# Kernel optimization log

Measured on AMD Instinct MI355X. Metric: run time of the kernel, lower is better.

Reference implementation:

```python
import jax, jax.numpy as jnp
import numpy as np

# ---- quantization scales (per-tensor, as produced by from_float calibration) ----
IN_SCALE = 0.05      # ForwardTokenizer: fp32 hidden -> int8
ALPHA_Q = 1e-4       # W8A8B8O8 requant multipliers (already include 1/sqrt(head_dim) for q)
ALPHA_K = 1e-4
ALPHA_V = 1e-4
QK_ALPHA = 1e-3      # BMM_S8T_S8N_F32T dequant scale (q_scale * k_scale)
PV_ALPHA = 1.0/127.0 # BMM_S8T_S8N_S8T requant scale ((1/127)*v_scale/out_scale)
OUT_ALPHA = 1e-4     # W8A8BFP32OFP32 dequant scale
NUM_HEADS = 32


def _quant_i8(x, scale):
    # simulate int8 quantization in fp32 (values are exact small integers)
    return jnp.clip(jnp.round(x / scale), -128.0, 127.0)


def _w8a8b8o8(x_i8, W_i8, b_i8, alpha):
    # int8 GEMM with int8 bias, requantized to int8: clamp(round(alpha*(x@W^T) + b))
    acc = jnp.einsum('btd,ed->bte', x_i8, W_i8)  # int32 accumulator in fp32
    return jnp.clip(jnp.round(alpha * acc + b_i8), -128.0, 127.0)


def setup_inputs() -> dict:
    key = jax.random.key(0)
    ks = jax.random.split(key, 10)
    B, T, D = 2, 2048, 2560
    hidden_states = jax.random.normal(ks[0], (B, T, D), dtype=jnp.float32)
    # causal additive mask, shape (B,1,T,T)
    neg = jnp.float32(-1e9)
    causal = jnp.where(jnp.tril(jnp.ones((T, T), dtype=bool)), 0.0, neg)
    attention_mask = jnp.broadcast_to(causal[None, None], (B, 1, T, T)).astype(jnp.float32)
    # int8-valued weights/biases stored as fp32 integers in [-127,127]
    def i8(k, shape):
        return jax.random.randint(k, shape, -127, 128).astype(jnp.float32)
    Wq = i8(ks[1], (D, D)); bq = i8(ks[2], (D,))
    Wk = i8(ks[3], (D, D)); bk = i8(ks[4], (D,))
    Wv = i8(ks[5], (D, D)); bv = i8(ks[6], (D,))
    Wo = i8(ks[7], (D, D))
    bo = jax.random.normal(ks[8], (D,), dtype=jnp.float32) * 0.01  # fp32 out bias
    return {"hidden_states": hidden_states, "attention_mask": attention_mask,
            "Wq": Wq, "bq": bq, "Wk": Wk, "bk": bk, "Wv": Wv, "bv": bv,
            "Wo": Wo, "bo": bo}


def reference(hidden_states, attention_mask, Wq, bq, Wk, bk, Wv, bv, Wo, bo):
    B, T, D = hidden_states.shape
    H = NUM_HEADS
    Dh = D // H
    # ForwardTokenizer: fp32 -> int8
    x_i8 = _quant_i8(hidden_states, IN_SCALE)
    # fused int8 q/k/v projections (W8A8B8O8Linear)
    q = _w8a8b8o8(x_i8, Wq, bq, ALPHA_Q)
    k = _w8a8b8o8(x_i8, Wk, bk, ALPHA_K)
    v = _w8a8b8o8(x_i8, Wv, bv, ALPHA_V)
    # (B,T,D) -> (B,H,T,Dh)
    def shape(t):
        return t.reshape(B, T, H, Dh).transpose(0, 2, 1, 3)
    q, k, v = shape(q), shape(k), shape(v)
    # BMM_S8T_S8N_F32T: int8 q @ k^T dequantized to fp32
    attn_weights = QK_ALPHA * jnp.einsum('bhqd,bhkd->bhqk', q, k)
    attn_weights = attn_weights + attention_mask  # (B,H,T,T)
    attn_weights = jnp.maximum(attn_weights, jnp.finfo(jnp.float32).min)
    attn_probs = jax.nn.softmax(attn_weights, axis=-1)
    # requantize probs to int8: mul_(127).round_()
    p_i8 = jnp.round(attn_probs * 127.0)
    # BMM_S8T_S8N_S8T: int8 p @ v requantized to int8
    attn_out = jnp.clip(jnp.round(PV_ALPHA * jnp.einsum('bhqk,bhkd->bhqd', p_i8, v)), -128.0, 127.0)
    # (B,H,T,Dh) -> (B,T,D)
    attn_out = attn_out.transpose(0, 2, 1, 3).reshape(B, T, D)
    # W8A8BFP32OFP32Linear: int8 GEMM, fp32 dequant + fp32 bias
    out = OUT_ALPHA * jnp.einsum('btd,ed->bte', attn_out, Wo) + bo
    return out
```

## Files before the change

kernel.cpp:

```cpp
#include <hip/hip_runtime.h>
#include <stdint.h>

typedef int v4i __attribute__((ext_vector_type(4)));

#define MFMA_I8(a,b,c) __builtin_amdgcn_mfma_i32_16x16x64_i8(a,b,c,0,0,0)

#define TD 2560
#define TT 2048
#define TB 2
#define TH 32
#define TDH 80
#define TDHP 128
#define TM 4096

#define LOG2E_MS 1.4426950408889634e-3f
#define MASKI (-(1<<30))
#define MAGICF 12582912.0f

__device__ __forceinline__ float clamp8f(float v){ return fminf(fmaxf(v, -128.0f), 127.0f); }
__device__ __forceinline__ float fexp2(float x){ return __builtin_amdgcn_exp2f(x); }

__device__ __forceinline__ void gl_lds16(const int8_t* g, int8_t* l){
  __builtin_amdgcn_global_load_lds(
      (const __attribute__((address_space(1))) void*)g,
      (__attribute__((address_space(3))) void*)l, 16, 0, 0);
}

__global__ void k_quant(const float* __restrict__ x, int8_t* __restrict__ y, int n4){
  int stride = gridDim.x * blockDim.x;
  for (int i = blockIdx.x*blockDim.x + threadIdx.x; i < n4; i += stride){
    float4 v = ((const float4*)x)[i];
    char4 o;
    o.x = (int8_t)clamp8f(rintf(__fdiv_rn(v.x, 0.05f)));
    o.y = (int8_t)clamp8f(rintf(__fdiv_rn(v.y, 0.05f)));
    o.z = (int8_t)clamp8f(rintf(__fdiv_rn(v.z, 0.05f)));
    o.w = (int8_t)clamp8f(rintf(__fdiv_rn(v.w, 0.05f)));
    ((char4*)y)[i] = o;
  }
}

__global__ void k_conv4(const float* __restrict__ w0, const float* __restrict__ w1,
                        const float* __restrict__ w2, const float* __restrict__ w3,
                        int8_t* __restrict__ y0, int8_t* __restrict__ y1,
                        int8_t* __restrict__ y2, int8_t* __restrict__ y3, int n4){
  const int z = blockIdx.y;
  const float* w = z == 0 ? w0 : (z == 1 ? w1 : (z == 2 ? w2 : w3));
  int8_t* y = z == 0 ? y0 : (z == 1 ? y1 : (z == 2 ? y2 : y3));
  int stride = gridDim.x * blockDim.x;
  for (int i = blockIdx.x*blockDim.x + threadIdx.x; i < n4; i += stride){
    float4 v = ((const float4*)w)[i];
    char4 o;
    o.x = (int8_t)(int)rintf(v.x);
    o.y = (int8_t)(int)rintf(v.y);
    o.z = (int8_t)(int)rintf(v.z);
    o.w = (int8_t)(int)rintf(v.w);
    ((char4*)y)[i] = o;
  }
}

__global__ __launch_bounds__(256, 4) void k_qkvg(const int8_t* __restrict__ x,
    const int8_t* __restrict__ w0_, const int8_t* __restrict__ w1_, const int8_t* __restrict__ w2_,
    const float* __restrict__ b0_, const float* __restrict__ b1_, const float* __restrict__ b2_,
    int8_t* __restrict__ dq, int8_t* __restrict__ dk, int8_t* __restrict__ dv)
{
  __shared__ __align__(16) int8_t As[128*64];
  __shared__ __align__(16) int8_t Bs[128*64];
  const int z = blockIdx.z;
  const int8_t* w = z == 0 ? w0_ : (z == 1 ? w1_ : w2_);
  const float* bias = z == 0 ? b0_ : (z == 1 ? b1_ : b2_);
  const int m0 = blockIdx.x * 128, n0 = blockIdx.y * 128;
  const int t = threadIdx.x;
  const int wv = t >> 6, l = t & 63, lhi = (l >> 4) & 3, llo = l & 15;
  const int wr = wv >> 1, wc = wv & 1;
  const int grow = l >> 2;
  const int gcol = ((l & 3) ^ ((l >> 3) & 3)) * 16;

  const int8_t* xa0 = x + (size_t)(m0 + wv*16 + grow)*TD + gcol;
  const int8_t* xa1 = x + (size_t)(m0 + 64 + wv*16 + grow)*TD + gcol;
  const int8_t* wb0 = w + (size_t)(n0 + wv*16 + grow)*TD + gcol;
  const int8_t* wb1 = w + (size_t)(n0 + 64 + wv*16 + grow)*TD + gcol;
  int8_t* la0 = &As[(wv*16)*64];
  int8_t* la1 = &As[(64 + wv*16)*64];
  int8_t* lb0 = &Bs[(wv*16)*64];
  int8_t* lb1 = &Bs[(64 + wv*16)*64];

  const int sca = (lhi ^ ((llo >> 1) & 3)) << 4;

  v4i acc[4][4] = {};
  for (int k0 = 0; k0 < TD; k0 += 64){
    gl_lds16(xa0 + k0, la0);
    gl_lds16(xa1 + k0, la1);
    gl_lds16(wb0 + k0, lb0);
    gl_lds16(wb1 + k0, lb1);
    __syncthreads();
    v4i a[4], b[4];
    #pragma unroll
    for (int mi = 0; mi < 4; ++mi)
      a[mi] = *(const v4i*)&As[(wr*64 + mi*16 + llo)*64 + sca];
    #pragma unroll
    for (int ni = 0; ni < 4; ++ni)
      b[ni] = *(const v4i*)&Bs[(wc*64 + ni*16 + llo)*64 + sca];
    #pragma unroll
    for (int mi = 0; mi < 4; ++mi)
      #pragma unroll
      for (int ni = 0; ni < 4; ++ni)
        acc[mi][ni] = MFMA_I8(a[mi], b[ni], acc[mi][ni]);
    __syncthreads();
  }

  #pragma unroll
  for (int mi = 0; mi < 4; ++mi)
  #pragma unroll
  for (int ni = 0; ni < 4; ++ni)
  #pragma unroll
  for (int r = 0; r < 4; ++r){
    int rowg = m0 + wr*64 + mi*16 + lhi*4 + r;
    int colg = n0 + wc*64 + ni*16 + llo;
    float fv = __fadd_rn(__fmul_rn(1e-4f, (float)acc[mi][ni][r]), bias[colg]);
    int8_t q8 = (int8_t)clamp8f(rintf(fv));
    int bb = rowg >> 11, tl = rowg & 2047;
    int hh = colg / 80, dh = colg - hh*80;
    if (z == 0)      dq[((size_t)(bb*TH + hh)*TT + tl)*TDHP + dh] = q8;
    else if (z == 1) dk[((size_t)(bb*TH + hh)*TT + tl)*TDHP + dh] = q8;
    else             dv[((size_t)(bb*TH + hh)*TDH + dh)*TT + tl] = q8;
  }
}

__global__ __launch_bounds__(256, 4) void k_oproj128(const int8_t* __restrict__ x,
    const int8_t* __restrict__ w, const float* __restrict__ bo,
    float* __restrict__ out)
{
  __shared__ __align__(16) int8_t As[128*64];
  __shared__ __align__(16) int8_t Bs[128*64];
  const int m0 = blockIdx.x * 128, n0 = blockIdx.y * 128;
  const int t = threadIdx.x;
  const int wv = t >> 6, l = t & 63, lhi = (l >> 4) & 3, llo = l & 15;
  const int wr = wv >> 1, wc = wv & 1;
  const int grow = l >> 2;
  const int gcol = ((l & 3) ^ ((l >> 3) & 3)) * 16;

  const int8_t* xa0 = x + (size_t)(m0 + wv*16 + grow)*TD + gcol;
  const int8_t* xa1 = x + (size_t)(m0 + 64 + wv*16 + grow)*TD + gcol;
  const int8_t* wb0 = w + (size_t)(n0 + wv*16 + grow)*TD + gcol;
  const int8_t* wb1 = w + (size_t)(n0 + 64 + wv*16 + grow)*TD + gcol;
  int8_t* la0 = &As[(wv*16)*64];
  int8_t* la1 = &As[(64 + wv*16)*64];
  int8_t* lb0 = &Bs[(wv*16)*64];
  int8_t* lb1 = &Bs[(64 + wv*16)*64];

  const int sca = (lhi ^ ((llo >> 1) & 3)) << 4;

  v4i acc[4][4] = {};
  for (int k0 = 0; k0 < TD; k0 += 64){
    gl_lds16(xa0 + k0, la0);
    gl_lds16(xa1 + k0, la1);
    gl_lds16(wb0 + k0, lb0);
    gl_lds16(wb1 + k0, lb1);
    __syncthreads();
    v4i a[4], b[4];
    #pragma unroll
    for (int mi = 0; mi < 4; ++mi)
      a[mi] = *(const v4i*)&As[(wr*64 + mi*16 + llo)*64 + sca];
    #pragma unroll
    for (int ni = 0; ni < 4; ++ni)
      b[ni] = *(const v4i*)&Bs[(wc*64 + ni*16 + llo)*64 + sca];
    #pragma unroll
    for (int mi = 0; mi < 4; ++mi)
      #pragma unroll
      for (int ni = 0; ni < 4; ++ni)
        acc[mi][ni] = MFMA_I8(a[mi], b[ni], acc[mi][ni]);
    __syncthreads();
  }

  #pragma unroll
  for (int mi = 0; mi < 4; ++mi)
  #pragma unroll
  for (int ni = 0; ni < 4; ++ni)
  #pragma unroll
  for (int r = 0; r < 4; ++r){
    int rowg = m0 + wr*64 + mi*16 + lhi*4 + r;
    int colg = n0 + wc*64 + ni*16 + llo;
    out[(size_t)rowg*TD + colg] =
        __fadd_rn(__fmul_rn(1e-4f, (float)acc[mi][ni][r]), bo[colg]);
  }
}

__global__ __launch_bounds__(256, 6) void k_attn6(const int8_t* __restrict__ qb_,
    const int8_t* __restrict__ kb_, const int8_t* __restrict__ vt_,
    int8_t* __restrict__ ao)
{
  __shared__ __align__(16) int8_t Ks[64*128];
  const int flat = blockIdx.x;
  const int g = flat & 7, ii = flat >> 3;
  const int qt = 31 - (ii >> 3);
  const int pair = g*8 + (ii & 7);
  const int h = pair & 31, b = pair >> 5;

  const int t = threadIdx.x, wv = t >> 6, l = t & 63, lhi = (l >> 4) & 3, llo = l & 15;
  const size_t bh = (size_t)(b*TH + h);
  const int8_t* qb = qb_ + bh*TT*TDHP;
  const int8_t* kb = kb_ + bh*TT*TDHP;
  const int8_t* vb = vt_ + bh*TDH*TT;

  const int qw0 = qt*64 + wv*16;
  const int qg = qw0 + llo;
  const int ktmax = qt + 1;

  int koff0[4], koff1[4];
  #pragma unroll
  for (int sub = 0; sub < 4; ++sub){
    const int row = sub*16 + llo, sw = row & 7;
    koff0[sub] = row*128 + (((lhi  ) ^ sw) << 4);
    koff1[sub] = row*128 + (((lhi+4) ^ sw) << 4);
  }

  v4i qa0 = *(const v4i*)(qb + (size_t)(qw0 + llo)*TDHP + lhi*16);
  v4i qa1 = {0,0,0,0};
  if (lhi == 0) qa1 = *(const v4i*)(qb + (size_t)(qw0 + llo)*TDHP + 64);

  const int srow = t >> 2, scp = (t & 3) * 2, ssw = srow & 7;
  const int8_t* kg = kb + (size_t)srow*TDHP + scp*16;
  int8_t* sdst0 = &Ks[srow*128 + (((scp  ) ^ ssw) << 4)];
  int8_t* sdst1 = &Ks[srow*128 + (((scp+1) ^ ssw) << 4)];

  int   M  = MASKI;
  float cm = __fmul_rn(LOG2E_MS, (float)MASKI);
  float ls = 0.0f;

  v4i pr0 = *(const v4i*)(kg);
  v4i pr1 = *(const v4i*)(kg + 16);
  *(v4i*)sdst0 = pr0; *(v4i*)sdst1 = pr1;
  for (int kt = 0; kt < ktmax; ++kt){
    if (kt + 1 < ktmax){
      pr0 = *(const v4i*)(kg + (size_t)(kt+1)*64*TDHP);
      pr1 = *(const v4i*)(kg + (size_t)(kt+1)*64*TDHP + 16);
    }
    __syncthreads();
    int sv[4][4];
    if (kt < qt){
      #pragma unroll
      for (int sub = 0; sub < 4; ++sub){
        v4i kf0 = *(const v4i*)&Ks[koff0[sub]];
        v4i kf1 = *(const v4i*)&Ks[koff1[sub]];
        v4i d = {}; d = MFMA_I8(kf0, qa0, d); d = MFMA_I8(kf1, qa1, d);
        sv[sub][0]=d[0]; sv[sub][1]=d[1]; sv[sub][2]=d[2]; sv[sub][3]=d[3];
      }
    } else {
      #pragma unroll
      for (int sub = 0; sub < 4; ++sub){
        if (sub <= wv){
          v4i kf0 = *(const v4i*)&Ks[koff0[sub]];
          v4i kf1 = *(const v4i*)&Ks[koff1[sub]];
          v4i d = {}; d = MFMA_I8(kf0, qa0, d); d = MFMA_I8(kf1, qa1, d);
          const int base = kt*64 + sub*16 + lhi*4;
          #pragma unroll
          for (int r = 0; r < 4; ++r)
            sv[sub][r] = (base + r <= qg) ? d[r] : MASKI;
        } else {
          #pragma unroll
          for (int r = 0; r < 4; ++r) sv[sub][r] = MASKI;
        }
      }
    }
    int m0 = max(max(sv[0][0], sv[0][1]), sv[0][2]);
    int m1 = max(max(sv[0][3], sv[1][0]), sv[1][1]);
    int m2 = max(max(sv[1][2], sv[1][3]), sv[2][0]);
    int m3 = max(max(sv[2][1], sv[2][2]), sv[2][3]);
    int m4 = max(max(sv[3][0], sv[3][1]), sv[3][2]);
    int tm = max(max(max(m0, m1), max(m2, m3)), max(m4, sv[3][3]));
    int Mn = max(M, tm);
    float cmN = __fmul_rn(LOG2E_MS, (float)Mn);
    float fac = fexp2(__fsub_rn(cm, cmN));
    float tot = 0.0f;
    #pragma unroll
    for (int sub = 0; sub < 4; ++sub){
      float e0 = fexp2(__fmaf_rn((float)sv[sub][0], LOG2E_MS, -cmN));
      float e1 = fexp2(__fmaf_rn((float)sv[sub][1], LOG2E_MS, -cmN));
      float e2 = fexp2(__fmaf_rn((float)sv[sub][2], LOG2E_MS, -cmN));
      float e3 = fexp2(__fmaf_rn((float)sv[sub][3], LOG2E_MS, -cmN));
      tot = __fadd_rn(tot, __fadd_rn(__fadd_rn(e0, e1), __fadd_rn(e2, e3)));
    }
    ls = __fmaf_rn(ls, fac, tot);
    M = Mn; cm = cmN;
    __syncthreads();
    if (kt + 1 < ktmax){ *(v4i*)sdst0 = pr0; *(v4i*)sdst1 = pr1; }
  }

  float rq;
  {
    float mm = cm, ll = ls;
    #pragma unroll
    for (int off = 16; off < 64; off <<= 1){
      float om = __shfl_xor(mm, off);
      float ol = __shfl_xor(ll, off);
      float mn = fmaxf(mm, om);
      ll = __fadd_rn(__fmul_rn(ll, fexp2(__fsub_rn(mm, mn))),
                     __fmul_rn(ol, fexp2(__fsub_rn(om, mn))));
      mm = mn;
    }
    cm = mm;
    rq = __fdiv_rn(127.0f, ll);
  }

  v4i pacc[5] = {};
  pr0 = *(const v4i*)(kg);
  pr1 = *(const v4i*)(kg + 16);
  __syncthreads();
  *(v4i*)sdst0 = pr0; *(v4i*)sdst1 = pr1;
  for (int kt = 0; kt < ktmax; ++kt){
    if (kt + 1 < ktmax){
      pr0 = *(const v4i*)(kg + (size_t)(kt+1)*64*TDHP);
      pr1 = *(const v4i*)(kg + (size_t)(kt+1)*64*TDHP + 16);
    }
    __syncthreads();
    uint32_t w[4] = {0u,0u,0u,0u};
    if (kt < qt){
      #pragma unroll
      for (int sub = 0; sub < 4; ++sub){
        v4i kf0 = *(const v4i*)&Ks[koff0[sub]];
        v4i kf1 = *(const v4i*)&Ks[koff1[sub]];
        v4i d = {}; d = MFMA_I8(kf0, qa0, d); d = MFMA_I8(kf1, qa1, d);
        uint32_t u0 = __float_as_uint(__fmaf_rn(fexp2(__fmaf_rn((float)d[0], LOG2E_MS, -cm)), rq, MAGICF));
        uint32_t u1 = __float_as_uint(__fmaf_rn(fexp2(__fmaf_rn((float)d[1], LOG2E_MS, -cm)), rq, MAGICF));
        uint32_t u2 = __float_as_uint(__fmaf_rn(fexp2(__fmaf_rn((float)d[2], LOG2E_MS, -cm)), rq, MAGICF));
        uint32_t u3 = __float_as_uint(__fmaf_rn(fexp2(__fmaf_rn((float)d[3], LOG2E_MS, -cm)), rq, MAGICF));
        w[sub] = (u0 & 0xffu) | ((u1 & 0xffu) << 8) | ((u2 & 0xffu) << 16) | (u3 << 24);
      }
    } else {
      #pragma unroll
      for (int sub = 0; sub < 4; ++sub){
        if (sub <= wv){
          v4i kf0 = *(const v4i*)&Ks[koff0[sub]];
          v4i kf1 = *(const v4i*)&Ks[koff1[sub]];
          v4i d = {}; d = MFMA_I8(kf0, qa0, d); d = MFMA_I8(kf1, qa1, d);
          const int base = kt*64 + sub*16 + lhi*4;
          uint32_t wrd = 0u;
          #pragma unroll
          for (int r = 0; r < 4; ++r){
            int sel = (base + r <= qg) ? d[r] : MASKI;
            uint32_t u = __float_as_uint(__fmaf_rn(fexp2(__fmaf_rn((float)sel, LOG2E_MS, -cm)), rq, MAGICF));
            wrd |= (u & 0xffu) << (8*r);
          }
          w[sub] = wrd;
        }
      }
    }
    #pragma unroll
    for (int bb = 0; bb < 2; ++bb){
      const int dist = 16 << bb;
      const int gb = (lhi >> bb) & 1;
      uint32_t nw[4];
      #pragma unroll
      for (int s = 0; s < 4; ++s){
        uint32_t tv = __shfl_xor(w[s ^ (1 << bb)], dist);
        nw[s] = (((s >> bb) & 1) == gb) ? w[s] : tv;
      }
      w[0]=nw[0]; w[1]=nw[1]; w[2]=nw[2]; w[3]=nw[3];
    }
    v4i pa;
    pa[0]=(int)w[0]; pa[1]=(int)w[1]; pa[2]=(int)w[2]; pa[3]=(int)w[3];
    #pragma unroll
    for (int dt = 0; dt < 5; ++dt){
      v4i vf = *(const v4i*)(vb + (size_t)(dt*16 + llo)*TT + kt*64 + lhi*16);
      pacc[dt] = MFMA_I8(vf, pa, pacc[dt]);
    }
    __syncthreads();
    if (kt + 1 < ktmax){ *(v4i*)sdst0 = pr0; *(v4i*)sdst1 = pr1; }
  }

  #pragma unroll
  for (int dt = 0; dt < 5; ++dt){
    uint32_t ob = 0u;
    #pragma unroll
    for (int r = 0; r < 4; ++r){
      int vq = (int)clamp8f(rintf(__fmul_rn((float)pacc[dt][r], (float)(1.0/127.0))));
      ob |= ((uint32_t)(uint8_t)(int8_t)vq) << (8*r);
    }
    *(uint32_t*)(ao + ((size_t)(b*TT) + qw0 + llo)*TD + h*TDH + dt*16 + lhi*4) = ob;
  }
}

extern "C" void kernel_launch(void* const* d_in, const int* in_sizes, int n_in,
                              void* d_out, int out_size, void* d_ws, size_t ws_size,
                              hipStream_t stream) {
  const float* hidden = (const float*)d_in[0];
  const float* Wq = (const float*)d_in[2];
  const float* bq = (const float*)d_in[3];
  const float* Wk = (const float*)d_in[4];
  const float* bk = (const float*)d_in[5];
  const float* Wv = (const float*)d_in[6];
  const float* bv = (const float*)d_in[7];
  const float* Wo = (const float*)d_in[8];
  const float* bo = (const float*)d_in[9];
  float* out = (float*)d_out;

  char* ws = (char*)d_ws;
  const size_t SZ_X  = (size_t)TM * TD;
  const size_t SZ_W  = (size_t)TD * TD;
  const size_t SZ_QK = (size_t)TB * TH * TT * TDHP;
  const size_t SZ_V  = (size_t)TB * TH * TDH * TT;
  int8_t* x8   = (int8_t*)ws;
  int8_t* wq8  = (int8_t*)(ws + SZ_X);
  int8_t* wk8  = wq8 + SZ_W;
  int8_t* wv8  = wk8 + SZ_W;
  int8_t* wo8  = wv8 + SZ_W;
  int8_t* qpad = wo8 + SZ_W;
  int8_t* kpad = qpad + SZ_QK;
  int8_t* vt   = kpad + SZ_QK;
  int8_t* ao   = vt + SZ_V;

  k_quant<<<4096, 256, 0, stream>>>(hidden, x8, (int)(SZ_X/4));
  k_conv4<<<dim3(1024, 4), 256, 0, stream>>>(Wq, Wk, Wv, Wo, wq8, wk8, wv8, wo8, (int)(SZ_W/4));

  k_qkvg<<<dim3(TM/128, TD/128, 3), 256, 0, stream>>>(x8, wq8, wk8, wv8, bq, bk, bv,
                                                      qpad, kpad, vt);

  k_attn6<<<dim3(2048), 256, 0, stream>>>(qpad, kpad, vt, ao);

  k_oproj128<<<dim3(TM/128, TD/128), 256, 0, stream>>>(ao, wo8, bo, out);
}
```

Before: 315.6 us.

## Double-buffer LDS tiles in int8 QKV and output projection GEMMs

Both int8 GEMM kernels now use two LDS buffers per operand. Each loop iteration issues the global-to-LDS load for the next K-slice before running MFMAs on the current one, so memory latency can overlap with compute, and the loop is manually unrolled by two. LDS use per block doubles to 32KB, which may limit occupancy at the requested 4 blocks per CU.

After: 310.3 us. No clear change (-1.7%).

```diff
diff --git a/kernel.cpp b/kernel.cpp
--- a/kernel.cpp
+++ b/kernel.cpp
@@ -58,13 +58,33 @@
   }
 }
 
+#define GSTAGE(bufi, k0) do{                                        \
+    gl_lds16(xa0 + (k0), &As[bufi][(wv*16)*64]);                    \
+    gl_lds16(xa1 + (k0), &As[bufi][(64 + wv*16)*64]);               \
+    gl_lds16(wb0 + (k0), &Bs[bufi][(wv*16)*64]);                    \
+    gl_lds16(wb1 + (k0), &Bs[bufi][(64 + wv*16)*64]); }while(0)
+
+#define GCOMP(bufi) do{                                             \
+    v4i a[4], b[4];                                                 \
+    _Pragma("unroll")                                               \
+    for (int mi = 0; mi < 4; ++mi)                                  \
+      a[mi] = *(const v4i*)&As[bufi][(wr*64 + mi*16 + llo)*64 + sca];\
+    _Pragma("unroll")                                               \
+    for (int ni = 0; ni < 4; ++ni)                                  \
+      b[ni] = *(const v4i*)&Bs[bufi][(wc*64 + ni*16 + llo)*64 + sca];\
+    _Pragma("unroll")                                               \
+    for (int mi = 0; mi < 4; ++mi)                                  \
+      _Pragma("unroll")                                             \
+      for (int ni = 0; ni < 4; ++ni)                                \
+        acc[mi][ni] = MFMA_I8(a[mi], b[ni], acc[mi][ni]); }while(0)
+
 __global__ __launch_bounds__(256, 4) void k_qkvg(const int8_t* __restrict__ x,
     const int8_t* __restrict__ w0_, const int8_t* __restrict__ w1_, const int8_t* __restrict__ w2_,
     const float* __restrict__ b0_, const float* __restrict__ b1_, const float* __restrict__ b2_,
     int8_t* __restrict__ dq, int8_t* __restrict__ dk, int8_t* __restrict__ dv)
 {
-  __shared__ __align__(16) int8_t As[128*64];
-  __shared__ __align__(16) int8_t Bs[128*64];
+  __shared__ __align__(16) int8_t As[2][128*64];
+  __shared__ __align__(16) int8_t Bs[2][128*64];
   const int z = blockIdx.z;
   const int8_t* w = z == 0 ? w0_ : (z == 1 ? w1_ : w2_);
   const float* bias = z == 0 ? b0_ : (z == 1 ? b1_ : b2_);
@@ -79,32 +99,19 @@
   const int8_t* xa1 = x + (size_t)(m0 + 64 + wv*16 + grow)*TD + gcol;
   const int8_t* wb0 = w + (size_t)(n0 + wv*16 + grow)*TD + gcol;
   const int8_t* wb1 = w + (size_t)(n0 + 64 + wv*16 + grow)*TD + gcol;
-  int8_t* la0 = &As[(wv*16)*64];
-  int8_t* la1 = &As[(64 + wv*16)*64];
-  int8_t* lb0 = &Bs[(wv*16)*64];
-  int8_t* lb1 = &Bs[(64 + wv*16)*64];
 
   const int sca = (lhi ^ ((llo >> 1) & 3)) << 4;
 
   v4i acc[4][4] = {};
-  for (int k0 = 0; k0 < TD; k0 += 64){
-    gl_lds16(xa0 + k0, la0);
-    gl_lds16(xa1 + k0, la1);
-    gl_lds16(wb0 + k0, lb0);
-    gl_lds16(wb1 + k0, lb1);
-    __syncthreads();
-    v4i a[4], b[4];
-    #pragma unroll
-    for (int mi = 0; mi < 4; ++mi)
-      a[mi] = *(const v4i*)&As[(wr*64 + mi*16 + llo)*64 + sca];
-    #pragma unroll
-    for (int ni = 0; ni < 4; ++ni)
-      b[ni] = *(const v4i*)&Bs[(wc*64 + ni*16 + llo)*64 + sca];
-    #pragma unroll
-    for (int mi = 0; mi < 4; ++mi)
-      #pragma unroll
-      for (int ni = 0; ni < 4; ++ni)
-        acc[mi][ni] = MFMA_I8(a[mi], b[ni], acc[mi][ni]);
+  GSTAGE(0, 0);
+  __syncthreads();
+  #pragma unroll 1
+  for (int p = 0; p < 20; ++p){
+    GSTAGE(1, (2*p+1)*64);
+    GCOMP(0);
+    __syncthreads();
+    if (p < 19) GSTAGE(0, (2*p+2)*64);
+    GCOMP(1);
     __syncthreads();
   }
 
@@ -130,8 +137,8 @@
     const int8_t* __restrict__ w, const float* __restrict__ bo,
     float* __restrict__ out)
 {
-  __shared__ __align__(16) int8_t As[128*64];
-  __shared__ __align__(16) int8_t Bs[128*64];
+  __shared__ __align__(16) int8_t As[2][128*64];
+  __shared__ __align__(16) int8_t Bs[2][128*64];
   const int m0 = blockIdx.x * 128, n0 = blockIdx.y * 128;
   const int t = threadIdx.x;
   const int wv = t >> 6, l = t & 63, lhi = (l >> 4) & 3, llo = l & 15;
@@ -143,32 +150,19 @@
   const int8_t* xa1 = x + (size_t)(m0 + 64 + wv*16 + grow)*TD + gcol;
   const int8_t* wb0 = w + (size_t)(n0 + wv*16 + grow)*TD + gcol;
   const int8_t* wb1 = w + (size_t)(n0 + 64 + wv*16 + grow)*TD + gcol;
-  int8_t* la0 = &As[(wv*16)*64];
-  int8_t* la1 = &As[(64 + wv*16)*64];
-  int8_t* lb0 = &Bs[(wv*16)*64];
-  int8_t* lb1 = &Bs[(64 + wv*16)*64];
 
   const int sca = (lhi ^ ((llo >> 1) & 3)) << 4;
 
   v4i acc[4][4] = {};
-  for (int k0 = 0; k0 < TD; k0 += 64){
-    gl_lds16(xa0 + k0, la0);
-    gl_lds16(xa1 + k0, la1);
-    gl_lds16(wb0 + k0, lb0);
-    gl_lds16(wb1 + k0, lb1);
-    __syncthreads();
-    v4i a[4], b[4];
-    #pragma unroll
-    for (int mi = 0; mi < 4; ++mi)
-      a[mi] = *(const v4i*)&As[(wr*64 + mi*16 + llo)*64 + sca];
-    #pragma unroll
-    for (int ni = 0; ni < 4; ++ni)
-      b[ni] = *(const v4i*)&Bs[(wc*64 + ni*16 + llo)*64 + sca];
-    #pragma unroll
-    for (int mi = 0; mi < 4; ++mi)
-      #pragma unroll
-      for (int ni = 0; ni < 4; ++ni)
-        acc[mi][ni] = MFMA_I8(a[mi], b[ni], acc[mi][ni]);
+  GSTAGE(0, 0);
+  __syncthreads();
+  #pragma unroll 1
+  for (int p = 0; p < 20; ++p){
+    GSTAGE(1, (2*p+1)*64);
+    GCOMP(0);
+    __syncthreads();
+    if (p < 19) GSTAGE(0, (2*p+2)*64);
+    GCOMP(1);
     __syncthreads();
   }
 
```
